# Kernel optimization log

Hardware: AMD Instinct MI355X
Metric: run time of the kernel (lower is better)

## Reference

```python
import jax, jax.numpy as jnp
import numpy as np

jax.config.update("jax_enable_x64", True)  # faithful int64 fixed-point requantize

B, K, N = 2048, 4096, 8192
INT32_MAX_MINUS = 2147418112  # threshold from multiply_by_quantize_mul


def setup_inputs() -> dict:
    key = jax.random.key(0)
    k1, k2, k3 = jax.random.split(key, 3)
    x = jax.random.randint(k1, (B, K), -128, 128, dtype=jnp.int8)
    weights = jax.random.randint(k2, (N, K), -128, 128, dtype=jnp.int8)
    bias = jax.random.randint(k3, (N, 1), -1024, 1024, dtype=jnp.int32)
    return {
        "x": x,
        "weights": weights,
        "bias": bias,
        "q_mantissa": 1431655765,   # ~2/3 in Q31 fixed point
        "exponent": -3,
        "output_zero_point": -5,
    }


def multiply_by_quantize_mul(x, q_mantissa, exponent):
    # Python precedence in original: (q_mantissa + (1<<15)) >> 16
    reduced_mantissa = ((q_mantissa + (1 << 15)) >> 16) if q_mantissa < INT32_MAX_MINUS else 32767
    total_shifts = 15 - exponent
    x = x * np.int64(reduced_mantissa)
    x = x + np.int64(1 << (total_shifts - 1))  # rounding term
    return jnp.right_shift(x, total_shifts)    # arithmetic shift on signed int64


def reference(x, weights, bias, q_mantissa, exponent, output_zero_point):
    # int8 GEMM accumulated in int32: result[b, n] = sum_k x[b, k] * w[n, k]
    acc = jnp.einsum("bk,nk->bn", x.astype(jnp.int32), weights.astype(jnp.int32))
    acc = acc + bias.T  # bias [N,1] -> [1,N], broadcast over batch
    acc = multiply_by_quantize_mul(acc.astype(jnp.int64), q_mantissa, exponent)
    acc = acc + np.int64(output_zero_point)
    out = jnp.clip(acc, -128, 127).astype(jnp.int8)
    return out
```

## Files before the change

kernel.cpp:

```cpp
#include <hip/hip_runtime.h>

#define DEVI __device__ __forceinline__

typedef int i32x4 __attribute__((ext_vector_type(4)));

static constexpr int Bdim = 2048;
static constexpr int Kdim = 4096;
static constexpr int Ndim = 8192;
static constexpr int BK   = 128;
static constexpr int NT   = Kdim / BK;

typedef __attribute__((address_space(1))) const unsigned int gas_t;
typedef __attribute__((address_space(3))) unsigned int las_t;

DEVI void gload_lds16(const void* g, void* l) {
    __builtin_amdgcn_global_load_lds((gas_t*)g, (las_t*)l, 16, 0, 0);
}

DEVI int pack4(i32x4 v) {
    return (v[0] & 255) | ((v[1] & 255) << 8) | ((v[2] & 255) << 16) | (v[3] << 24);
}

__global__ void pack_i32_to_i8(const int* __restrict__ in, char* __restrict__ out, int n16) {
    int i = blockIdx.x * blockDim.x + threadIdx.x;
    if (i >= n16) return;
    const i32x4* src = (const i32x4*)in + (size_t)i * 4;
    i32x4 r;
    r[0] = pack4(src[0]);
    r[1] = pack4(src[1]);
    r[2] = pack4(src[2]);
    r[3] = pack4(src[3]);
    ((i32x4*)out)[i] = r;
}

#define CFENCE asm volatile("" ::: "memory")
DEVI void bar() { CFENCE; __builtin_amdgcn_s_barrier(); CFENCE; }
#define WAITVM(N) asm volatile("s_waitcnt vmcnt(" #N ")" ::: "memory")
#define PRIO1 __builtin_amdgcn_s_setprio(1)
#define PRIO0 __builtin_amdgcn_s_setprio(0)

#define QUAD(MB)                                                                 \
    do {                                                                         \
        _Pragma("unroll") for (int mm = 0; mm < 4; ++mm)                         \
        _Pragma("unroll") for (int n = 0; n < 4; ++n)                            \
            acc[(MB) + mm][n] = __builtin_amdgcn_mfma_i32_16x16x64_i8(           \
                a[mm], b[n], acc[(MB) + mm][n], 0, 0, 0);                        \
    } while (0)

#define TILE(T, CUR, S1, S2, S3, S4, VM)                                         \
    {                                                                            \
        _Pragma("unroll") for (int mm = 0; mm < 4; ++mm) a[mm] = rdA(CUR, 0, mm);\
        _Pragma("unroll") for (int n = 0; n < 4; ++n)    b[n]  = rdB(CUR, 0, n); \
        S1; bar(); PRIO1; QUAD(0); PRIO0; bar();                                 \
        _Pragma("unroll") for (int mm = 0; mm < 4; ++mm) a[mm] = rdA(CUR, 0, 4 + mm); \
        S2; bar(); PRIO1; QUAD(4); PRIO0; bar();                                 \
        _Pragma("unroll") for (int mm = 0; mm < 4; ++mm) a[mm] = rdA(CUR, 1, mm);\
        _Pragma("unroll") for (int n = 0; n < 4; ++n)    b[n]  = rdB(CUR, 1, n); \
        S3; bar(); PRIO1; QUAD(0); PRIO0; bar();                                 \
        _Pragma("unroll") for (int mm = 0; mm < 4; ++mm) a[mm] = rdA(CUR, 1, 4 + mm); \
        S4; bar(); PRIO1; QUAD(4); PRIO0; VM; bar();                             \
    }

__global__ __launch_bounds__(512, 2)
void gemm8(const char* __restrict__ A8, const char* __restrict__ B8,
           const int* __restrict__ bias,
           const int* __restrict__ qm_p, const int* __restrict__ ex_p,
           const int* __restrict__ zp_p, int* __restrict__ out) {
    __shared__ __align__(16) char smem[131072];

    const int tid  = threadIdx.x;
    const int wid  = tid >> 6;
    const int lane = tid & 63;
    const int l15  = lane & 15;
    const int lks  = lane >> 4;
    const int wr   = wid >> 2;
    const int wc   = wid & 3;

    const int bid = blockIdx.x;
    const int swz = (bid & 7) * 32 + (bid >> 3);
    const int bm  = swz >> 5;
    const int bn  = swz & 31;
    const int arow0 = bm * 256;
    const int brow0 = bn * 256;

    const int sw16 = (lks ^ ((l15 >> 1) & 3)) * 16;
    const int a_rd = (wr * 128 + l15) * 64 + sw16;
    const int b_rd = 65536 + (wc * 64 + l15) * 64 + sw16;

    const int st_c = (tid & 3) ^ ((tid >> 3) & 3);
    const char* agp = A8 + (size_t)(arow0 + (tid >> 2)) * Kdim + st_c * 16;
    const char* bgp = B8 + (size_t)(brow0 + (tid >> 2)) * Kdim + st_c * 16;

    auto stage = [&](int isb, int t, int ks) {
        const char* gp = (isb ? bgp : agp) + (size_t)t * BK + ks * 64;
        const int lb = (isb ? 65536 : 0) + (t & 1) * 32768 + ks * 16384 + tid * 16;
        gload_lds16(gp, &smem[lb]);
        gload_lds16(gp + (size_t)128 * Kdim, &smem[lb + 8192]);
    };
    auto rdA = [&](int buf, int ks, int m) {
        return *(const i32x4*)&smem[buf * 32768 + ks * 16384 + a_rd + m * 1024];
    };
    auto rdB = [&](int buf, int ks, int n) {
        return *(const i32x4*)&smem[buf * 32768 + ks * 16384 + b_rd + n * 1024];
    };

    i32x4 acc[8][4] = {};
    i32x4 a[4], b[4];

    stage(1, 0, 0); stage(0, 0, 0); stage(1, 0, 1); stage(0, 0, 1);
    stage(1, 1, 0); stage(0, 1, 0); stage(1, 1, 1);
    WAITVM(6);
    bar();

    int cur = 0;
    for (int t = 0; t < NT - 2; ++t) {
        TILE(t, cur,
             stage(0, t + 1, 1),
             stage(1, t + 2, 0),
             stage(0, t + 2, 0),
             stage(1, t + 2, 1),
             WAITVM(6));
        cur ^= 1;
    }
    TILE(NT - 2, cur,
         stage(0, NT - 1, 1),
         ((void)0), ((void)0), ((void)0),
         WAITVM(0));
    cur ^= 1;
    TILE(NT - 1, cur, ((void)0), ((void)0), ((void)0), ((void)0), ((void)0));

    const int qm = *qm_p;
    const int ex = *ex_p;
    const int zp = *zp_p;
    const int rm = (qm < 2147418112) ? ((qm + (1 << 15)) >> 16) : 32767;
    const int shifts = 15 - ex;
    const long long rnd = (shifts > 0) ? (1LL << (shifts - 1)) : 0;

    int bv[4];
#pragma unroll
    for (int n = 0; n < 4; ++n) bv[n] = bias[brow0 + wc * 64 + n * 16 + l15];

#pragma unroll
    for (int m = 0; m < 8; ++m) {
        const int row0 = arow0 + wr * 128 + m * 16 + lks * 4;
#pragma unroll
        for (int n = 0; n < 4; ++n) {
            const int col = brow0 + wc * 64 + n * 16 + l15;
#pragma unroll
            for (int j = 0; j < 4; ++j) {
                long long t = (long long)(acc[m][n][j] + bv[n]) * rm + rnd;
                t >>= shifts;
                t += zp;
                t = t < -128 ? -128 : (t > 127 ? 127 : t);
                out[(size_t)(row0 + j) * Ndim + col] = (int)t;
            }
        }
    }
}

extern "C" void kernel_launch(void* const* d_in, const int* in_sizes, int n_in,
                              void* d_out, int out_size, void* d_ws, size_t ws_size,
                              hipStream_t stream) {
    const int* x32  = (const int*)d_in[0];
    const int* w32  = (const int*)d_in[1];
    const int* bias = (const int*)d_in[2];
    const int* qm   = (const int*)d_in[3];
    const int* ex   = (const int*)d_in[4];
    const int* zp   = (const int*)d_in[5];
    int* out = (int*)d_out;

    char* xa = (char*)d_ws;
    char* wa = xa + (size_t)Bdim * Kdim;
    const int nx16 = Bdim * Kdim / 16;
    const int nw16 = Ndim * Kdim / 16;
    pack_i32_to_i8<<<(nx16 + 255) / 256, 256, 0, stream>>>(x32, xa, nx16);
    pack_i32_to_i8<<<(nw16 + 255) / 256, 256, 0, stream>>>(w32, wa, nw16);

    const int grid = (Bdim / 256) * (Ndim / 256);
    gemm8<<<grid, 512, 0, stream>>>(xa, wa, bias, qm, ex, zp, out);
}
```

Before: 107.8 us.

## Replace 256x256 GEMM with 128x256 tile using 32x32x32 MFMA and simpler double buffer

Replaces the hand-scheduled 256x256-tile, BK=128 kernel with a 128x256 tile, BK=64 kernel. It uses 32x32x32 int8 MFMAs, a smaller LDS footprint (48KB) so four blocks can fit per CU, and a plain double-buffered loop synchronised with __syncthreads. The aim is higher occupancy and simpler scheduling. In exchange it gives up the barrier/priority interleaving, the explicit vmcnt waits, and some data reuse per block.

```diff
diff --git a/kernel.cpp b/kernel.cpp
--- a/kernel.cpp
+++ b/kernel.cpp
@@ -2,12 +2,13 @@
 
 #define DEVI __device__ __forceinline__
 
-typedef int i32x4 __attribute__((ext_vector_type(4)));
+typedef int i32x4  __attribute__((ext_vector_type(4)));
+typedef int i32x16 __attribute__((ext_vector_type(16)));
 
 static constexpr int Bdim = 2048;
 static constexpr int Kdim = 4096;
 static constexpr int Ndim = 8192;
-static constexpr int BK   = 128;
+static constexpr int BK   = 64;
 static constexpr int NT   = Kdim / BK;
 
 typedef __attribute__((address_space(1))) const unsigned int gas_t;
@@ -33,101 +34,90 @@
     ((i32x4*)out)[i] = r;
 }
 
-#define CFENCE asm volatile("" ::: "memory")
-DEVI void bar() { CFENCE; __builtin_amdgcn_s_barrier(); CFENCE; }
-#define WAITVM(N) asm volatile("s_waitcnt vmcnt(" #N ")" ::: "memory")
-#define PRIO1 __builtin_amdgcn_s_setprio(1)
-#define PRIO0 __builtin_amdgcn_s_setprio(0)
-
-#define QUAD(MB)                                                                 \
-    do {                                                                         \
-        _Pragma("unroll") for (int mm = 0; mm < 4; ++mm)                         \
-        _Pragma("unroll") for (int n = 0; n < 4; ++n)                            \
-            acc[(MB) + mm][n] = __builtin_amdgcn_mfma_i32_16x16x64_i8(           \
-                a[mm], b[n], acc[(MB) + mm][n], 0, 0, 0);                        \
-    } while (0)
-
-#define TILE(T, CUR, S1, S2, S3, S4, VM)                                         \
-    {                                                                            \
-        _Pragma("unroll") for (int mm = 0; mm < 4; ++mm) a[mm] = rdA(CUR, 0, mm);\
-        _Pragma("unroll") for (int n = 0; n < 4; ++n)    b[n]  = rdB(CUR, 0, n); \
-        S1; bar(); PRIO1; QUAD(0); PRIO0; bar();                                 \
-        _Pragma("unroll") for (int mm = 0; mm < 4; ++mm) a[mm] = rdA(CUR, 0, 4 + mm); \
-        S2; bar(); PRIO1; QUAD(4); PRIO0; bar();                                 \
-        _Pragma("unroll") for (int mm = 0; mm < 4; ++mm) a[mm] = rdA(CUR, 1, mm);\
-        _Pragma("unroll") for (int n = 0; n < 4; ++n)    b[n]  = rdB(CUR, 1, n); \
-        S3; bar(); PRIO1; QUAD(0); PRIO0; bar();                                 \
-        _Pragma("unroll") for (int mm = 0; mm < 4; ++mm) a[mm] = rdA(CUR, 1, 4 + mm); \
-        S4; bar(); PRIO1; QUAD(4); PRIO0; VM; bar();                             \
-    }
-
-__global__ __launch_bounds__(512, 2)
-void gemm8(const char* __restrict__ A8, const char* __restrict__ B8,
-           const int* __restrict__ bias,
-           const int* __restrict__ qm_p, const int* __restrict__ ex_p,
-           const int* __restrict__ zp_p, int* __restrict__ out) {
-    __shared__ __align__(16) char smem[131072];
+__global__ __launch_bounds__(512, 4)
+void gemm2b(const char* __restrict__ A8, const char* __restrict__ B8,
+            const int* __restrict__ bias,
+            const int* __restrict__ qm_p, const int* __restrict__ ex_p,
+            const int* __restrict__ zp_p, int* __restrict__ out) {
+    __shared__ __align__(16) char smem[49152];
 
     const int tid  = threadIdx.x;
     const int wid  = tid >> 6;
     const int lane = tid & 63;
-    const int l15  = lane & 15;
-    const int lks  = lane >> 4;
+    const int l31  = lane & 31;
+    const int hc   = lane >> 5;
     const int wr   = wid >> 2;
     const int wc   = wid & 3;
 
     const int bid = blockIdx.x;
-    const int swz = (bid & 7) * 32 + (bid >> 3);
+    const int swz = (bid & 7) * 64 + (bid >> 3);
     const int bm  = swz >> 5;
     const int bn  = swz & 31;
-    const int arow0 = bm * 256;
+    const int arow0 = bm * 128;
     const int brow0 = bn * 256;
-
-    const int sw16 = (lks ^ ((l15 >> 1) & 3)) * 16;
-    const int a_rd = (wr * 128 + l15) * 64 + sw16;
-    const int b_rd = 65536 + (wc * 64 + l15) * 64 + sw16;
 
     const int st_c = (tid & 3) ^ ((tid >> 3) & 3);
     const char* agp = A8 + (size_t)(arow0 + (tid >> 2)) * Kdim + st_c * 16;
     const char* bgp = B8 + (size_t)(brow0 + (tid >> 2)) * Kdim + st_c * 16;
 
-    auto stage = [&](int isb, int t, int ks) {
-        const char* gp = (isb ? bgp : agp) + (size_t)t * BK + ks * 64;
-        const int lb = (isb ? 65536 : 0) + (t & 1) * 32768 + ks * 16384 + tid * 16;
-        gload_lds16(gp, &smem[lb]);
-        gload_lds16(gp + (size_t)128 * Kdim, &smem[lb + 8192]);
-    };
-    auto rdA = [&](int buf, int ks, int m) {
-        return *(const i32x4*)&smem[buf * 32768 + ks * 16384 + a_rd + m * 1024];
-    };
-    auto rdB = [&](int buf, int ks, int n) {
-        return *(const i32x4*)&smem[buf * 32768 + ks * 16384 + b_rd + n * 1024];
+    auto stage = [&](int t) {
+        const int buf = (t & 1) * 24576;
+        gload_lds16(agp + (size_t)t * BK, &smem[buf + tid * 16]);
+        gload_lds16(bgp + (size_t)t * BK, &smem[buf + 8192 + tid * 16]);
+        gload_lds16(bgp + (size_t)128 * Kdim + (size_t)t * BK,
+                    &smem[buf + 8192 + 8192 + tid * 16]);
     };
 
-    i32x4 acc[8][4] = {};
-    i32x4 a[4], b[4];
+    int aoff[2][2], boff[2][2];
+#pragma unroll
+    for (int m = 0; m < 2; ++m) {
+        const int row = wr * 64 + m * 32 + l31;
+        const int xr  = (row >> 1) & 3;
+#pragma unroll
+        for (int s = 0; s < 2; ++s)
+            aoff[s][m] = row * 64 + (((s * 2 + hc) ^ xr)) * 16;
+    }
+#pragma unroll
+    for (int n = 0; n < 2; ++n) {
+        const int row = wc * 64 + n * 32 + l31;
+        const int xr  = (row >> 1) & 3;
+#pragma unroll
+        for (int s = 0; s < 2; ++s)
+            boff[s][n] = 8192 + row * 64 + (((s * 2 + hc) ^ xr)) * 16;
+    }
 
-    stage(1, 0, 0); stage(0, 0, 0); stage(1, 0, 1); stage(0, 0, 1);
-    stage(1, 1, 0); stage(0, 1, 0); stage(1, 1, 1);
-    WAITVM(6);
-    bar();
+    i32x16 acc[2][2] = {};
 
-    int cur = 0;
-    for (int t = 0; t < NT - 2; ++t) {
-        TILE(t, cur,
-             stage(0, t + 1, 1),
-             stage(1, t + 2, 0),
-             stage(0, t + 2, 0),
-             stage(1, t + 2, 1),
-             WAITVM(6));
-        cur ^= 1;
+    auto compute = [&](int t) {
+        const int buf = (t & 1) * 24576;
+        i32x4 a[2][2], b[2][2];
+#pragma unroll
+        for (int s = 0; s < 2; ++s)
+#pragma unroll
+            for (int m = 0; m < 2; ++m)
+                a[s][m] = *(const i32x4*)&smem[buf + aoff[s][m]];
+#pragma unroll
+        for (int s = 0; s < 2; ++s)
+#pragma unroll
+            for (int n = 0; n < 2; ++n)
+                b[s][n] = *(const i32x4*)&smem[buf + boff[s][n]];
+#pragma unroll
+        for (int m = 0; m < 2; ++m)
+#pragma unroll
+            for (int n = 0; n < 2; ++n)
+#pragma unroll
+                for (int s = 0; s < 2; ++s)
+                    acc[m][n] = __builtin_amdgcn_mfma_i32_32x32x32_i8(
+                        a[s][m], b[s][n], acc[m][n], 0, 0, 0);
+    };
+
+    stage(0);
+    __syncthreads();
+    for (int t = 0; t < NT; ++t) {
+        if (t + 1 < NT) stage(t + 1);
+        compute(t);
+        __syncthreads();
     }
-    TILE(NT - 2, cur,
-         stage(0, NT - 1, 1),
-         ((void)0), ((void)0), ((void)0),
-         WAITVM(0));
-    cur ^= 1;
-    TILE(NT - 1, cur, ((void)0), ((void)0), ((void)0), ((void)0), ((void)0));
 
     const int qm = *qm_p;
     const int ex = *ex_p;
@@ -136,23 +126,24 @@
     const int shifts = 15 - ex;
     const long long rnd = (shifts > 0) ? (1LL << (shifts - 1)) : 0;
 
-    int bv[4];
+    int bv[2];
 #pragma unroll
-    for (int n = 0; n < 4; ++n) bv[n] = bias[brow0 + wc * 64 + n * 16 + l15];
+    for (int n = 0; n < 2; ++n) bv[n] = bias[brow0 + wc * 64 + n * 32 + l31];
 
 #pragma unroll
-    for (int m = 0; m < 8; ++m) {
-        const int row0 = arow0 + wr * 128 + m * 16 + lks * 4;
+    for (int m = 0; m < 2; ++m) {
+        const int rbase = arow0 + wr * 64 + m * 32 + hc * 4;
 #pragma unroll
-        for (int n = 0; n < 4; ++n) {
-            const int col = brow0 + wc * 64 + n * 16 + l15;
+        for (int n = 0; n < 2; ++n) {
+            const int col = brow0 + wc * 64 + n * 32 + l31;
 #pragma unroll
-            for (int j = 0; j < 4; ++j) {
+            for (int j = 0; j < 16; ++j) {
+                const int row = rbase + (j & 3) + (j >> 2) * 8;
                 long long t = (long long)(acc[m][n][j] + bv[n]) * rm + rnd;
                 t >>= shifts;
                 t += zp;
                 t = t < -128 ? -128 : (t > 127 ? 127 : t);
-                out[(size_t)(row0 + j) * Ndim + col] = (int)t;
+                out[(size_t)row * Ndim + col] = (int)t;
             }
         }
     }
@@ -176,6 +167,6 @@
     pack_i32_to_i8<<<(nx16 + 255) / 256, 256, 0, stream>>>(x32, xa, nx16);
     pack_i32_to_i8<<<(nw16 + 255) / 256, 256, 0, stream>>>(w32, wa, nw16);
 
-    const int grid = (Bdim / 256) * (Ndim / 256);
-    gemm8<<<grid, 512, 0, stream>>>(xa, wa, bias, qm, ex, zp, out);
+    const int grid = (Bdim / 128) * (Ndim / 256);
+    gemm2b<<<grid, 512, 0, stream>>>(xa, wa, bias, qm, ex, zp, out);
 }
```

Result: slower. 119.5 us (+10.8%).
